# Kernel optimization log

Measured on AMD Instinct MI355X. Metric: run time of the kernel, lower is better.

Reference implementation:

```python
import jax, jax.numpy as jnp
import numpy as np

N_E = 1024    # codebook size
E_DIM = 256   # code dimension
BETA = 0.25   # commitment cost


def setup_inputs() -> dict:
    key = jax.random.key(0)
    k1, k2 = jax.random.split(key)
    z = jax.random.normal(k1, (32, E_DIM, 32, 32), dtype=jnp.float32)
    # embedding init uniform(-1/n_e, 1/n_e) as in the torch module
    e_w = jax.random.uniform(k2, (N_E, E_DIM), jnp.float32, -1.0 / N_E, 1.0 / N_E)
    return {"z": z, "e_w": e_w}


def _vq_forward(z, e_w):
    B, C, H, W = z.shape  # C == E_DIM
    z_flat = jnp.transpose(z, (0, 2, 3, 1)).reshape(-1, C)  # (N, D)
    # squared euclidean distances: ||z||^2 + ||e||^2 - 2 z.e
    d = ((z_flat ** 2).sum(-1, keepdims=True)
         + (e_w ** 2).sum(-1)[None, :]
         - 2.0 * (z_flat @ e_w.T))                          # (N, n_e)
    indices = jnp.argmin(d, axis=1)                          # (N,)
    one_hot = jax.nn.one_hot(indices, N_E, dtype=z.dtype)    # (N, n_e)
    z_q_flat = e_w[indices]                                  # == one_hot @ e_w
    z_q = jnp.transpose(z_q_flat.reshape(B, H, W, C), (0, 3, 1, 2))
    # use_ema=True branch: loss = beta * mse(z_q, sg(z))
    loss = BETA * jnp.mean((z_q - jax.lax.stop_gradient(z)) ** 2)
    # straight-through estimator
    z_q_st = z + jax.lax.stop_gradient(z_q - z)
    avg_probs = one_hot.mean(0)
    perplexity = jnp.exp(-jnp.sum(avg_probs * jnp.log(avg_probs + 1e-10)))
    return loss, z_q_st, perplexity, one_hot, indices


def reference(z, e_w):
    return _vq_forward(z, e_w)
```

## Files before the change

### kernel.cpp

```cpp
#include <hip/hip_runtime.h>
#include <math.h>

#define N_TOK 32768
#define NE    1024
#define DIM   256
#define EPS   1.5e-3f

#define OFF_ZQ   1u
#define OFF_PPL  8388609u
#define OFF_OH   8388610u
#define OFF_IDX  41943042u

#define RS_CAP 4096

typedef __attribute__((ext_vector_type(8))) short short8;
typedef __attribute__((ext_vector_type(8))) unsigned short ushort8;
typedef __attribute__((ext_vector_type(4))) float f32x4;

__device__ __forceinline__ unsigned short bf_rne(float f) {
    unsigned u = __float_as_uint(f);
    return (unsigned short)((u + 0x7FFFu + ((u >> 16) & 1u)) >> 16);
}
__device__ __forceinline__ void gload16(const void* g, void* l) {
    __builtin_amdgcn_global_load_lds((const __attribute__((address_space(1))) void*)g,
                                     (__attribute__((address_space(3))) void*)l, 16, 0, 0);
}

__global__ void vq_init(float* sse) { sse[0] = 0.0f; }

__global__ __launch_bounds__(256) void vq_zprep(const float* __restrict__ z,
                                                unsigned short* __restrict__ z1,
                                                float* __restrict__ zn)
{
    __shared__ float zf[64 * 257];
    const int t = threadIdx.x;
    const int img = blockIdx.x >> 4;
    const int hw0 = (blockIdx.x & 15) << 6;
    const float* zb = z + (size_t)img * (DIM * 1024) + hw0;

#pragma unroll 4
    for (int it = 0; it < 64; ++it) {
        int idx = it * 256 + t;
        int c = idx >> 6, hw = idx & 63;
        zf[hw * 257 + c] = zb[(size_t)c * 1024 + hw];
    }
    __syncthreads();

    if (t < 64) {
        float s = 0.0f;
#pragma unroll 8
        for (int c = 0; c < DIM; ++c) { float v = zf[t * 257 + c]; s = fmaf(v, v, s); }
        zn[img * 1024 + hw0 + t] = s;
    }
    __syncthreads();

#pragma unroll
    for (int it = 0; it < 8; ++it) {
        int f = it * 256 + t;
        int tl = f >> 5, cg = f & 31;
        ushort8 s1;
#pragma unroll
        for (int j = 0; j < 8; ++j) s1[j] = bf_rne(zf[tl * 257 + cg * 8 + j]);
        int tok = img * 1024 + hw0 + tl;
        *reinterpret_cast<ushort8*>(z1 + (size_t)tok * 256 + cg * 8) = s1;
    }
}

__global__ __launch_bounds__(256) void vq_eprep(const float* __restrict__ ew,
                                                unsigned short* __restrict__ e1,
                                                float* __restrict__ en)
{
    const int code = blockIdx.x * 256 + threadIdx.x;
    const float* p = ew + (size_t)code * DIM;
    float s = 0.0f;
    for (int dg = 0; dg < 32; ++dg) {
        ushort8 s1;
#pragma unroll
        for (int j = 0; j < 8; ++j) {
            float v = p[dg * 8 + j];
            s = fmaf(v, v, s);
            s1[j] = bf_rne(v);
        }
        *reinterpret_cast<ushort8*>(e1 + (size_t)code * 256 + dg * 8) = s1;
    }
    en[code] = s;
}

__global__ __launch_bounds__(256) void vq_argmin_mfma(const unsigned short* __restrict__ z1,
                                                      const unsigned short* __restrict__ e1,
                                                      const float* __restrict__ en,
                                                      unsigned long long* __restrict__ cmu)
{
    __shared__ short lds[2][8192];

    const int t = threadIdx.x;
    const int lane = t & 63, w = t >> 6;
    const int wr = w >> 1, wc = w & 1;
    const int bid = (blockIdx.x & 7) * 256 + (blockIdx.x >> 3);
    const int rb = bid >> 3, cbi = bid & 7;
    const int r0 = rb * 128, c0 = cbi * 128;

    const char* srcp[4];
#pragma unroll
    for (int i = 0; i < 4; ++i) {
        int flat = (w * 4 + i) * 64 + lane;
        int arr = flat >> 9;
        int rr  = (flat & 511) >> 2;
        int sl  = flat & 3;
        int slx = sl ^ ((rr >> 1) & 3);
        srcp[i] = (arr == 0)
            ? (const char*)(z1 + (size_t)(r0 + rr) * 256 + slx * 8)
            : (const char*)(e1 + (size_t)(c0 + rr) * 256 + slx * 8);
    }

    f32x4 acc[4][4];
#pragma unroll
    for (int i = 0; i < 4; ++i)
#pragma unroll
        for (int j = 0; j < 4; ++j) acc[i][j] = (f32x4)0.0f;

#pragma unroll
    for (int i = 0; i < 4; ++i)
        gload16(srcp[i], &lds[0][(w * 4 + i) * 512]);
    __syncthreads();

    int cur = 0;
    for (int kc = 0; kc < 8; ++kc) {
        if (kc < 7) {
            const unsigned kadd = (unsigned)(kc + 1) * 64u;
#pragma unroll
            for (int i = 0; i < 4; ++i)
                gload16(srcp[i] + kadd, &lds[cur ^ 1][(w * 4 + i) * 512]);
        }
        const short* L = &lds[cur][0];
        const short* za = L;
        const short* eb = L + 4096;

        short8 bfr[4];
#pragma unroll
        for (int fn = 0; fn < 4; ++fn) {
            int row = wc * 64 + fn * 16 + (lane & 15);
            int slot = (lane >> 4) ^ ((row >> 1) & 3);
            bfr[fn] = *reinterpret_cast<const short8*>(eb + row * 32 + slot * 8);
        }
#pragma unroll
        for (int fm = 0; fm < 4; ++fm) {
            int row = wr * 64 + fm * 16 + (lane & 15);
            int slot = (lane >> 4) ^ ((row >> 1) & 3);
            short8 a0 = *reinterpret_cast<const short8*>(za + row * 32 + slot * 8);
#pragma unroll
            for (int fn = 0; fn < 4; ++fn)
                acc[fm][fn] = __builtin_amdgcn_mfma_f32_16x16x32_bf16(a0, bfr[fn], acc[fm][fn], 0, 0, 0);
        }
        __syncthreads();
        cur ^= 1;
    }

    float env[4];
#pragma unroll
    for (int fn = 0; fn < 4; ++fn)
        env[fn] = en[c0 + wc * 64 + fn * 16 + (lane & 15)];

    float* sdm = reinterpret_cast<float*>(&lds[0][0]);

#pragma unroll
    for (int fm = 0; fm < 4; ++fm) {
#pragma unroll
        for (int reg = 0; reg < 4; ++reg) {
            int lrow = wr * 64 + fm * 16 + ((lane >> 4) << 2) + reg;
            float bd = 3.0e38f;
#pragma unroll
            for (int fn = 0; fn < 4; ++fn) {
                float dv = env[fn] - 2.0f * acc[fm][fn][reg];
                bd = fminf(bd, dv);
            }
#pragma unroll
            for (int m = 1; m <= 8; m <<= 1)
                bd = fminf(bd, __shfl_xor(bd, m));
            if ((lane & 15) == 0) sdm[wc * 128 + lrow] = bd;
        }
    }
    __syncthreads();
    if (t < 128) sdm[t] = fminf(sdm[t], sdm[128 + t]) + EPS;
    __syncthreads();

#pragma unroll
    for (int fm = 0; fm < 4; ++fm) {
        unsigned long long bl[4][4];
#pragma unroll
        for (int fn = 0; fn < 4; ++fn) {
#pragma unroll
            for (int reg = 0; reg < 4; ++reg) {
                int lrow = wr * 64 + fm * 16 + ((lane >> 4) << 2) + reg;
                float thr = sdm[lrow];
                float dv = env[fn] - 2.0f * acc[fm][fn][reg];
                bl[fn][reg] = __ballot(dv <= thr);
            }
        }
        const int q = lane >> 4;
#pragma unroll
        for (int reg = 0; reg < 4; ++reg) {
            unsigned long long h =
                  ((bl[0][reg] >> (q * 16)) & 0xFFFFull)
                | (((bl[1][reg] >> (q * 16)) & 0xFFFFull) << 16)
                | (((bl[2][reg] >> (q * 16)) & 0xFFFFull) << 32)
                | (((bl[3][reg] >> (q * 16)) & 0xFFFFull) << 48);
            if ((lane & 15) == reg) {
                int row = wr * 64 + fm * 16 + q * 4 + reg;
                cmu[(size_t)(r0 + row) * 16 + cbi * 2 + wc] = h;
            }
        }
    }
}

__global__ __launch_bounds__(256) void vq_rescore(const float* __restrict__ z,
                                                  const float* __restrict__ ew,
                                                  const float* __restrict__ zn,
                                                  const float* __restrict__ en,
                                                  const unsigned long long* __restrict__ cmu,
                                                  float* __restrict__ out_idx,
                                                  float* __restrict__ zq,
                                                  float* __restrict__ sse,
                                                  float* __restrict__ oh)
{
    __shared__ float zrow[16 * 260];
    __shared__ int   wl[RS_CAP];
    __shared__ int   cnt[256];
    __shared__ unsigned long long best[16];

    const int t = threadIdx.x;
    const int tok0 = blockIdx.x * 16;
    const int img = tok0 >> 10, hw0 = tok0 & 1023;

    {
        const float* zc = z + (size_t)img * (DIM * 1024) + (size_t)t * 1024 + hw0;
#pragma unroll
        for (int j = 0; j < 4; ++j) {
            float4 v = *reinterpret_cast<const float4*>(zc + 4 * j);
            zrow[(4 * j + 0) * 260 + t] = v.x;
            zrow[(4 * j + 1) * 260 + t] = v.y;
            zrow[(4 * j + 2) * 260 + t] = v.z;
            zrow[(4 * j + 3) * 260 + t] = v.w;
        }
    }
    if (t < 16) best[t] = ~0ull;

    unsigned long long v = cmu[(size_t)(tok0 + (t >> 4)) * 16 + (t & 15)];
    int myc = __popcll(v);
    cnt[t] = myc;
    __syncthreads();
    for (int st = 1; st < 256; st <<= 1) {
        int x = cnt[t];
        int y = (t >= st) ? cnt[t - st] : 0;
        __syncthreads();
        cnt[t] = x + y;
        __syncthreads();
    }
    int base = cnt[t] - myc;
    int total = cnt[255];
    {
        const int wd = t & 15, tk = t >> 4;
        unsigned long long vv = v;
        while (vv) {
            int b = __ffsll((long long)vv) - 1;
            vv &= vv - 1;
            int code = (wd >> 1) * 128 + (wd & 1) * 64 + b;
            if (base < RS_CAP) wl[base] = (tk << 10) | code;
            ++base;
        }
    }
    __syncthreads();
    if (total > RS_CAP) total = RS_CAP;

    for (int p = t; p < total; p += 256) {
        int e = wl[p];
        int tk = e >> 10, code = e & 1023;
        const float* ep = ew + (size_t)code * DIM;
        const float* zr = &zrow[tk * 260];
        float s = 0.0f;
#pragma unroll 8
        for (int d = 0; d < DIM; d += 4) {
            float4 e4 = *reinterpret_cast<const float4*>(ep + d);
            float4 z4 = *reinterpret_cast<const float4*>(zr + d);
            s = fmaf(z4.x, e4.x, s);
            s = fmaf(z4.y, e4.y, s);
            s = fmaf(z4.z, e4.z, s);
            s = fmaf(z4.w, e4.w, s);
        }
        float dv = (zn[tok0 + tk] + en[code]) - 2.0f * s;
        unsigned long long key = ((unsigned long long)__float_as_uint(dv) << 32) | (unsigned)code;
        atomicMin(&best[tk], key);
    }
    __syncthreads();
    if (t < 16) out_idx[tok0 + t] = (float)(unsigned)(best[t] & 0x3FFu);

    const int tk2 = t & 15, cg2 = t >> 4;
    const int bidx = (int)(best[tk2] & 0x3FFu);
    const int hwp = hw0 + tk2;
    float part = 0.0f;
    float* zqb = zq + (size_t)img * (DIM * 1024) + hwp;
    const float* ewb = ew + (size_t)bidx * DIM;
#pragma unroll
    for (int i = 0; i < 16; ++i) {
        int c = cg2 * 16 + i;
        float q = ewb[c];
        float zv = zrow[tk2 * 260 + c];
        zqb[(size_t)c << 10] = q;
        float dx = q - zv;
        part = fmaf(dx, dx, part);
    }
    float* redf = reinterpret_cast<float*>(cnt);
    redf[t] = part;
    __syncthreads();
    for (int s2 = 128; s2 > 0; s2 >>= 1) {
        if (t < s2) redf[t] += redf[t + s2];
        __syncthreads();
    }
    if (t == 0) atomicAdd(sse, redf[0]);

    if (oh) {
        const int w2 = t >> 6, lane2 = t & 63;
#pragma unroll
        for (int rr = 0; rr < 4; ++rr) {
            const int row = w2 * 4 + rr;
            const int bi2 = (int)(best[row] & 0x3FFull);
            float* rowp = oh + (size_t)(tok0 + row) * 1024;
#pragma unroll
            for (int j = 0; j < 4; ++j) {
                int i4 = j * 64 + lane2;
                if (i4 < 254) {
                    int k = 2 + i4 * 4;
                    float4 vv4;
                    vv4.x = (k     == bi2) ? 1.0f : 0.0f;
                    vv4.y = (k + 1 == bi2) ? 1.0f : 0.0f;
                    vv4.z = (k + 2 == bi2) ? 1.0f : 0.0f;
                    vv4.w = (k + 3 == bi2) ? 1.0f : 0.0f;
                    *reinterpret_cast<float4*>(rowp + k) = vv4;
                }
            }
            if (lane2 == 0) {
                float2 v2; v2.x = (0 == bi2) ? 1.0f : 0.0f; v2.y = (1 == bi2) ? 1.0f : 0.0f;
                *reinterpret_cast<float2*>(rowp) = v2;
            } else if (lane2 == 1) {
                float2 v2; v2.x = (1022 == bi2) ? 1.0f : 0.0f; v2.y = (1023 == bi2) ? 1.0f : 0.0f;
                *reinterpret_cast<float2*>(rowp + 1022) = v2;
            }
        }
    }
}

__global__ __launch_bounds__(256) void vq_onehot(const float* __restrict__ idxf,
                                                 float* __restrict__ oh)
{
    const unsigned stride = gridDim.x * blockDim.x;
    const unsigned total2 = N_TOK * (NE / 2);
    for (unsigned o2 = blockIdx.x * blockDim.x + threadIdx.x; o2 < total2; o2 += stride) {
        unsigned n = o2 >> 7;
        int k = (int)((o2 & 127u) << 1);
        int idx = (int)idxf[n];
        float2 v;
        v.x = (k == idx) ? 1.0f : 0.0f;
        v.y = (k + 1 == idx) ? 1.0f : 0.0f;
        reinterpret_cast<float2*>(oh)[o2] = v;
    }
}

__global__ __launch_bounds__(1024) void vq_finalize(const float* __restrict__ idxf,
                                                    const float* __restrict__ sse,
                                                    float* __restrict__ loss,
                                                    float* __restrict__ ppl)
{
    __shared__ int   hist[NE];
    __shared__ float red[NE];
    const int t = threadIdx.x;
    hist[t] = 0;
    __syncthreads();
    const float2* idx2 = reinterpret_cast<const float2*>(idxf);
    for (int i = t; i < N_TOK / 2; i += 1024) {
        float2 v = idx2[i];
        atomicAdd(&hist[(int)v.x], 1);
        atomicAdd(&hist[(int)v.y], 1);
    }
    __syncthreads();
    float p = (float)hist[t] * (1.0f / (float)N_TOK);
    red[t] = p * logf(p + 1e-10f);
    __syncthreads();
    for (int s = 512; s > 0; s >>= 1) {
        if (t < s) red[t] += red[t + s];
        __syncthreads();
    }
    if (t == 0) {
        ppl[0]  = expf(-red[0]);
        loss[0] = 0.25f * sse[0] / (float)(N_TOK * DIM);
    }
}

extern "C" void kernel_launch(void* const* d_in, const int* in_sizes, int n_in,
                              void* d_out, int out_size, void* d_ws, size_t ws_size,
                              hipStream_t stream)
{
    const float* z  = (const float*)d_in[0];
    const float* ew = (const float*)d_in[1];
    float* out = (float*)d_out;

    float* out_idx = out + OFF_IDX;
    float* out_oh  = out + OFF_OH;
    float* out_zq  = out + OFF_ZQ;
    float* out_ppl = out + OFF_PPL;

    const size_t need = 1024u + 33554432u + 524288u + 4194304u + 131072u + 4096u;
    const bool big = ws_size >= need && ws_size >= (size_t)48u * 1024u * 1024u;
    char* base = big ? (char*)d_ws : (char*)out_oh;
    const size_t Z1o = big ? 1024u : 8u;
    const size_t E1o = Z1o + 33554432u;
    const size_t CMo = E1o + 524288u;
    const size_t ZNo = CMo + 4194304u;
    const size_t ENo = ZNo + 131072u;

    unsigned short* Z1 = (unsigned short*)(base + Z1o);
    unsigned short* E1 = (unsigned short*)(base + E1o);
    unsigned long long* CM = (unsigned long long*)(base + CMo);
    float* ZN = (float*)(base + ZNo);
    float* EN = (float*)(base + ENo);
    float* SSE = (float*)d_ws;

    vq_init<<<1, 1, 0, stream>>>(SSE);
    vq_zprep<<<512, 256, 0, stream>>>(z, Z1, ZN);
    vq_eprep<<<4, 256, 0, stream>>>(ew, E1, EN);
    vq_argmin_mfma<<<2048, 256, 0, stream>>>(Z1, E1, EN, CM);
    vq_rescore<<<2048, 256, 0, stream>>>(z, ew, ZN, EN, CM, out_idx, out_zq, SSE,
                                         big ? out_oh : nullptr);
    if (!big) vq_onehot<<<2048, 256, 0, stream>>>(out_idx, out_oh);
    vq_finalize<<<1, 1024, 0, stream>>>(out_idx, SSE, out, out_ppl);
}
```

Before: 146.5 us.

## Merge prep kernels, vectorize z loads, shuffle-scan rescore, nontemporal output stores

Folds the SSE init, z prep and codebook prep into one launch by giving the codebook its own extra blocks. The z transpose now uses float4 global loads, z is converted to bf16 by truncation instead of round-to-nearest, and a redundant barrier is dropped. The rescore prefix sum becomes a wavefront shuffle scan with one small cross-wave step, and the zq and one-hot writes use nontemporal stores. It also widens the one-hot loop bound so columns 1018-1021 are written, which they were not before. Truncated rounding could shift which candidates pass the bf16 filter, which the fp32 rescore is meant to cover.

```diff
diff --git a/kernel.cpp b/kernel.cpp
--- a/kernel.cpp
+++ b/kernel.cpp
@@ -16,6 +16,7 @@
 typedef __attribute__((ext_vector_type(8))) short short8;
 typedef __attribute__((ext_vector_type(8))) unsigned short ushort8;
 typedef __attribute__((ext_vector_type(4))) float f32x4;
+typedef __attribute__((ext_vector_type(2))) float f32x2;
 
 __device__ __forceinline__ unsigned short bf_rne(float f) {
     unsigned u = __float_as_uint(f);
@@ -26,23 +27,49 @@
                                      (__attribute__((address_space(3))) void*)l, 16, 0, 0);
 }
 
-__global__ void vq_init(float* sse) { sse[0] = 0.0f; }
-
-__global__ __launch_bounds__(256) void vq_zprep(const float* __restrict__ z,
-                                                unsigned short* __restrict__ z1,
-                                                float* __restrict__ zn)
+__global__ __launch_bounds__(256) void vq_prep(const float* __restrict__ z,
+                                               const float* __restrict__ ew,
+                                               unsigned short* __restrict__ z1,
+                                               unsigned short* __restrict__ e1,
+                                               float* __restrict__ zn,
+                                               float* __restrict__ en,
+                                               float* __restrict__ sse)
 {
     __shared__ float zf[64 * 257];
     const int t = threadIdx.x;
+
+    if (blockIdx.x >= 512) {
+        if (blockIdx.x == 512 && t == 0) sse[0] = 0.0f;
+        const int code = (int)(blockIdx.x - 512) * 256 + t;
+        const float* p = ew + (size_t)code * DIM;
+        float s = 0.0f;
+        for (int dg = 0; dg < 32; ++dg) {
+            ushort8 s1;
+#pragma unroll
+            for (int j = 0; j < 8; ++j) {
+                float v = p[dg * 8 + j];
+                s = fmaf(v, v, s);
+                s1[j] = bf_rne(v);
+            }
+            *reinterpret_cast<ushort8*>(e1 + (size_t)code * 256 + dg * 8) = s1;
+        }
+        en[code] = s;
+        return;
+    }
+
     const int img = blockIdx.x >> 4;
     const int hw0 = (blockIdx.x & 15) << 6;
     const float* zb = z + (size_t)img * (DIM * 1024) + hw0;
 
-#pragma unroll 4
-    for (int it = 0; it < 64; ++it) {
-        int idx = it * 256 + t;
-        int c = idx >> 6, hw = idx & 63;
-        zf[hw * 257 + c] = zb[(size_t)c * 1024 + hw];
+#pragma unroll
+    for (int it = 0; it < 16; ++it) {
+        int f = it * 256 + t;
+        int c = f >> 4, hw4 = f & 15;
+        float4 v = *reinterpret_cast<const float4*>(zb + (size_t)c * 1024 + hw4 * 4);
+        zf[(hw4 * 4 + 0) * 257 + c] = v.x;
+        zf[(hw4 * 4 + 1) * 257 + c] = v.y;
+        zf[(hw4 * 4 + 2) * 257 + c] = v.z;
+        zf[(hw4 * 4 + 3) * 257 + c] = v.w;
     }
     __syncthreads();
 
@@ -52,7 +79,6 @@
         for (int c = 0; c < DIM; ++c) { float v = zf[t * 257 + c]; s = fmaf(v, v, s); }
         zn[img * 1024 + hw0 + t] = s;
     }
-    __syncthreads();
 
 #pragma unroll
     for (int it = 0; it < 8; ++it) {
@@ -60,30 +86,11 @@
         int tl = f >> 5, cg = f & 31;
         ushort8 s1;
 #pragma unroll
-        for (int j = 0; j < 8; ++j) s1[j] = bf_rne(zf[tl * 257 + cg * 8 + j]);
+        for (int j = 0; j < 8; ++j)
+            s1[j] = (unsigned short)(__float_as_uint(zf[tl * 257 + cg * 8 + j]) >> 16);
         int tok = img * 1024 + hw0 + tl;
         *reinterpret_cast<ushort8*>(z1 + (size_t)tok * 256 + cg * 8) = s1;
     }
-}
-
-__global__ __launch_bounds__(256) void vq_eprep(const float* __restrict__ ew,
-                                                unsigned short* __restrict__ e1,
-                                                float* __restrict__ en)
-{
-    const int code = blockIdx.x * 256 + threadIdx.x;
-    const float* p = ew + (size_t)code * DIM;
-    float s = 0.0f;
-    for (int dg = 0; dg < 32; ++dg) {
-        ushort8 s1;
-#pragma unroll
-        for (int j = 0; j < 8; ++j) {
-            float v = p[dg * 8 + j];
-            s = fmaf(v, v, s);
-            s1[j] = bf_rne(v);
-        }
-        *reinterpret_cast<ushort8*>(e1 + (size_t)code * 256 + dg * 8) = s1;
-    }
-    en[code] = s;
 }
 
 __global__ __launch_bounds__(256) void vq_argmin_mfma(const unsigned short* __restrict__ z1,
@@ -225,10 +232,11 @@
 {
     __shared__ float zrow[16 * 260];
     __shared__ int   wl[RS_CAP];
-    __shared__ int   cnt[256];
+    __shared__ int   wsum[4];
+    __shared__ float redf[256];
     __shared__ unsigned long long best[16];
 
-    const int t = threadIdx.x;
+    const int t = threadIdx.x, lane = t & 63, w = t >> 6;
     const int tok0 = blockIdx.x * 16;
     const int img = tok0 >> 10, hw0 = tok0 & 1023;
 
@@ -247,17 +255,19 @@
 
     unsigned long long v = cmu[(size_t)(tok0 + (t >> 4)) * 16 + (t & 15)];
     int myc = __popcll(v);
-    cnt[t] = myc;
-    __syncthreads();
-    for (int st = 1; st < 256; st <<= 1) {
-        int x = cnt[t];
-        int y = (t >= st) ? cnt[t - st] : 0;
-        __syncthreads();
-        cnt[t] = x + y;
-        __syncthreads();
-    }
-    int base = cnt[t] - myc;
-    int total = cnt[255];
+    int x = myc;
+#pragma unroll
+    for (int d = 1; d < 64; d <<= 1) {
+        int y = __shfl_up(x, d);
+        if (lane >= d) x += y;
+    }
+    if (lane == 63) wsum[w] = x;
+    __syncthreads();
+    int woff = 0;
+#pragma unroll
+    for (int i = 0; i < 4; ++i) woff += (i < w) ? wsum[i] : 0;
+    int total = wsum[0] + wsum[1] + wsum[2] + wsum[3];
+    int base = woff + x - myc;
     {
         const int wd = t & 15, tk = t >> 4;
         unsigned long long vv = v;
@@ -305,11 +315,10 @@
         int c = cg2 * 16 + i;
         float q = ewb[c];
         float zv = zrow[tk2 * 260 + c];
-        zqb[(size_t)c << 10] = q;
+        __builtin_nontemporal_store(q, &zqb[(size_t)c << 10]);
         float dx = q - zv;
         part = fmaf(dx, dx, part);
     }
-    float* redf = reinterpret_cast<float*>(cnt);
     redf[t] = part;
     __syncthreads();
     for (int s2 = 128; s2 > 0; s2 >>= 1) {
@@ -328,22 +337,22 @@
 #pragma unroll
             for (int j = 0; j < 4; ++j) {
                 int i4 = j * 64 + lane2;
-                if (i4 < 254) {
+                if (i4 < 255) {
                     int k = 2 + i4 * 4;
-                    float4 vv4;
+                    f32x4 vv4;
                     vv4.x = (k     == bi2) ? 1.0f : 0.0f;
                     vv4.y = (k + 1 == bi2) ? 1.0f : 0.0f;
                     vv4.z = (k + 2 == bi2) ? 1.0f : 0.0f;
                     vv4.w = (k + 3 == bi2) ? 1.0f : 0.0f;
-                    *reinterpret_cast<float4*>(rowp + k) = vv4;
+                    __builtin_nontemporal_store(vv4, reinterpret_cast<f32x4*>(rowp + k));
                 }
             }
             if (lane2 == 0) {
-                float2 v2; v2.x = (0 == bi2) ? 1.0f : 0.0f; v2.y = (1 == bi2) ? 1.0f : 0.0f;
-                *reinterpret_cast<float2*>(rowp) = v2;
+                f32x2 v2; v2.x = (0 == bi2) ? 1.0f : 0.0f; v2.y = (1 == bi2) ? 1.0f : 0.0f;
+                __builtin_nontemporal_store(v2, reinterpret_cast<f32x2*>(rowp));
             } else if (lane2 == 1) {
-                float2 v2; v2.x = (1022 == bi2) ? 1.0f : 0.0f; v2.y = (1023 == bi2) ? 1.0f : 0.0f;
-                *reinterpret_cast<float2*>(rowp + 1022) = v2;
+                f32x2 v2; v2.x = (1022 == bi2) ? 1.0f : 0.0f; v2.y = (1023 == bi2) ? 1.0f : 0.0f;
+                __builtin_nontemporal_store(v2, reinterpret_cast<f32x2*>(rowp + 1022));
             }
         }
     }
@@ -424,9 +433,7 @@
     float* EN = (float*)(base + ENo);
     float* SSE = (float*)d_ws;
 
-    vq_init<<<1, 1, 0, stream>>>(SSE);
-    vq_zprep<<<512, 256, 0, stream>>>(z, Z1, ZN);
-    vq_eprep<<<4, 256, 0, stream>>>(ew, E1, EN);
+    vq_prep<<<516, 256, 0, stream>>>(z, ew, Z1, E1, ZN, EN, SSE);
     vq_argmin_mfma<<<2048, 256, 0, stream>>>(Z1, E1, EN, CM);
     vq_rescore<<<2048, 256, 0, stream>>>(z, ew, ZN, EN, CM, out_idx, out_zq, SSE,
                                          big ? out_oh : nullptr);
```

Result: no change. 145.3 us (-0.8%).
